# Optimization experiments

Measured on AMD Instinct MI355X. Metric: run time of the kernel, lower is better.

## Reference

```python
import jax, jax.numpy as jnp
import numpy as np
from jax import lax

# --- constants derived from init args ---
TAU = 0.1
CNSTS = (1.0, 10.0)
EPSILON = CNSTS[0] / TAU          # 10.0
LAMBDAA = CNSTS[0] * CNSTS[1] / TAU  # 100.0
ALPHA = 0.5
SIGMA = 2.0
ITER_NUM = 5
IN_CHANNELS = 3
M = max(4 * int(2 * SIGMA) + 1, 5)  # 17


def gauss_kernel():
    # 2D normalized Gaussian, shape [C, 1, M, M] for depthwise conv (OIHW with groups=C)
    xx = jnp.arange(M, dtype=jnp.float32) - (M - 1.0) / 2.0
    d2 = xx[:, None] ** 2 + xx[None, :] ** 2
    w = jnp.exp(-d2 / (2.0 * SIGMA ** 2))
    w = w / w.sum()
    return jnp.broadcast_to(w[None, None], (IN_CHANNELS, 1, M, M))


def depthwise_conv(x, w):
    # x: [B, C, H, W], w: [C, 1, M, M]; SAME padding (M odd, pad = M//2)
    return lax.conv_general_dilated(
        x, w, window_strides=(1, 1), padding='SAME',
        dimension_numbers=('NCHW', 'OIHW', 'NCHW'),
        feature_group_count=IN_CHANNELS)


def setup_inputs() -> dict:
    key = jax.random.key(0)
    k1, k2 = jax.random.split(key)
    x = jax.random.uniform(k1, (8, 3, 512, 512), dtype=jnp.float32)
    c = jax.random.normal(k2, (8, 3, 512, 512), dtype=jnp.float32)
    return {'x': x, 'c': c}


def reference(x, c):
    w = gauss_kernel()
    b = jax.nn.sigmoid(10.0 * c)          # getb(c)
    lam_b = LAMBDAA * b
    u = jax.nn.sigmoid(-(lam_b * depthwise_conv(1.0 - 2.0 * x, w)) / EPSILON)
    for _ in range(max(abs(ITER_NUM), 1)):
        uu = (u - x) / TAU + lam_b * depthwise_conv(1.0 - 2.0 * u, w)
        uu = jax.nn.sigmoid(-uu / EPSILON)
        u = (1.0 - ALPHA) * u + ALPHA * uu
    return u
```

## Files before the change

kernel.cpp:

```cpp
#include <hip/hip_runtime.h>
#include <hip/hip_fp16.h>
#include <math.h>


#define TR   32
#define TC   64
#define HR   48
#define RAD  8
#define HW   512
#define NIMG 24
#define NPIX ((size_t)HW * HW * NIMG)

typedef _Float16 h2 __attribute__((ext_vector_type(2)));
typedef unsigned int uint;

#define G0  6.6916e-05f
#define G1  4.3635e-04f
#define G2  2.2159612e-03f
#define G3  8.7643070e-03f
#define G4  2.6995958e-02f
#define G5  6.4759932e-02f
#define G6  1.2098751e-01f
#define G7  1.7603572e-01f
#define G8  1.9947466e-01f
__device__ __constant__ const float GWc[17] = {
    G0,G1,G2,G3,G4,G5,G6,G7,G8,G7,G6,G5,G4,G3,G2,G1,G0
};

__device__ __forceinline__ float inv1pexp(float z) {
    return __builtin_amdgcn_rcpf(1.0f + __expf(z));
}

__device__ __forceinline__ float fdot2f(uint a, h2 b, float c) {
#if __has_builtin(__builtin_amdgcn_fdot2)
    return __builtin_amdgcn_fdot2(__builtin_bit_cast(h2, a), b, c, false);
#else
    h2 av = __builtin_bit_cast(h2, a);
    return (float)av.x * (float)b.x + (float)av.y * (float)b.y + c;
#endif
}
__device__ __forceinline__ float lo16f(uint v) {
    __half h = __ushort_as_half((unsigned short)(v & 0xffffu));
    return __half2float(h);
}
__device__ __forceinline__ float hi16f(uint v) {
    __half h = __ushort_as_half((unsigned short)(v >> 16));
    return __half2float(h);
}
__device__ __forceinline__ h2 gpair(int i) {
    const float G[16] = { G0,G1,G2,G3,G4,G5,G6,G7,G8,G7,G6,G5,G4,G3,G2,G1 };
    h2 r; r.x = (_Float16)G[2*i]; r.y = (_Float16)G[2*i+1]; return r;
}

template<int MODE>
__global__ __launch_bounds__(256, 6) void sig_step(
    const float* __restrict__ xg, const float* __restrict__ cgl,
    const __half* __restrict__ uin, __half2* __restrict__ xl,
    void* __restrict__ uout)
{
    __shared__ __half sTmp[HR * TC];

    const int t    = threadIdx.x;
    const int img  = blockIdx.z;
    const int row0 = blockIdx.y * TR;
    const int col0 = blockIdx.x * TC;
    const size_t ibase = (size_t)img * HW * HW;

    if (t < 192) {
        const int r   = t >> 2;
        const int ci2 = t & 3;
        const int gr  = row0 + r - RAD;
        const int gc0 = col0 + ci2 * 16 - RAD;

        uint wv[16];
#pragma unroll
        for (int i = 0; i < 16; ++i) wv[i] = 0x38003800u;
        if (gr >= 0 && gr < HW) {
            if constexpr (MODE == 0) {
#pragma unroll
                for (int k = 0; k < 4; ++k) {
                    int s = gc0 + 8 * k;
                    if (s >= 0 && s < HW) {
                        const float* xb = xg + ibase + (size_t)gr * HW + s;
                        float4 va = *reinterpret_cast<const float4*>(xb);
                        float4 vb = *reinterpret_cast<const float4*>(xb + 4);
                        wv[4*k+0] = __builtin_bit_cast(uint, __floats2half2_rn(va.x, va.y));
                        wv[4*k+1] = __builtin_bit_cast(uint, __floats2half2_rn(va.z, va.w));
                        wv[4*k+2] = __builtin_bit_cast(uint, __floats2half2_rn(vb.x, vb.y));
                        wv[4*k+3] = __builtin_bit_cast(uint, __floats2half2_rn(vb.z, vb.w));
                    }
                }
            } else {
#pragma unroll
                for (int k = 0; k < 4; ++k) {
                    int s = gc0 + 8 * k;
                    if (s >= 0 && s < HW) {
                        uint4 v = *reinterpret_cast<const uint4*>(
                                      uin + ibase + (size_t)gr * HW + s);
                        wv[4*k+0] = v.x; wv[4*k+1] = v.y;
                        wv[4*k+2] = v.z; wv[4*k+3] = v.w;
                    }
                }
            }
        }
        uint wo[15];
#pragma unroll
        for (int i = 0; i < 15; ++i)
            wo[i] = __builtin_amdgcn_alignbit(wv[i + 1], wv[i], 16);

        uint ow[8];
#pragma unroll
        for (int jp = 0; jp < 8; ++jp) {
            float a0 = 0.f, a1 = 0.f;
#pragma unroll
            for (int i = 0; i < 8; ++i) {
                h2 g = gpair(i);
                a0 = fdot2f(wv[jp + i], g, a0);
                a1 = fdot2f(wo[jp + i], g, a1);
            }
            a0 = fmaf(G0, lo16f(wv[jp + 8]), a0);
            a1 = fmaf(G0, hi16f(wv[jp + 8]), a1);
            ow[jp] = __builtin_bit_cast(uint, __floats2half2_rn(a0, a1));
        }
        uint4* orow = reinterpret_cast<uint4*>(&sTmp[r * TC + ci2 * 16]);
        orow[0] = make_uint4(ow[0], ow[1], ow[2], ow[3]);
        orow[1] = make_uint4(ow[4], ow[5], ow[6], ow[7]);
    }
    __syncthreads();

    const int cc = t & 63;
    const int rg = t >> 6;
    const size_t pbase = ibase + (size_t)(row0 + rg * 8) * HW + (col0 + cc);

    float win[24];
#pragma unroll
    for (int j = 0; j < 24; ++j)
        win[j] = __half2float(sTmp[(rg * 8 + j) * TC + cc]);

#pragma unroll
    for (int m = 0; m < 8; ++m) {
        float v = 0.f;
#pragma unroll
        for (int k = 0; k < 17; ++k) v += GWc[k] * win[m + k];
        float f = 1.f - 2.f * v;

        size_t gidx = pbase + (size_t)m * HW;
        if constexpr (MODE == 0) {
            float xv  = xg[gidx];
            float lam = 100.f * inv1pexp(-10.f * cgl[gidx]);
            xl[gidx] = __floats2half2_rn(xv, lam);
            ((__half*)uout)[gidx] = __float2half(inv1pexp(lam * f * 0.1f));
        } else {
            float2 p = __half22float2(xl[gidx]);
            float uprev = __half2float(uin[gidx]);
            float tt = (uprev - p.x) * 10.f + p.y * f;
            float uu = inv1pexp(tt * 0.1f);
            float res = 0.5f * (uprev + uu);
            if constexpr (MODE == 2) ((float*)uout)[gidx] = res;
            else                     ((__half*)uout)[gidx] = __float2half(res);
        }
    }
}

extern "C" void kernel_launch(void* const* d_in, const int* in_sizes, int n_in,
                              void* d_out, int out_size, void* d_ws, size_t ws_size,
                              hipStream_t stream) {
    const float* x = (const float*)d_in[0];
    const float* c = (const float*)d_in[1];

    __half* u0 = (__half*)d_ws;
    __half* u1 = u0 + NPIX;
    __half2* xl = (ws_size >= NPIX * 8)
        ? (__half2*)((char*)d_ws + NPIX * 4)
        : (__half2*)d_out;

    dim3 grid(HW / TC, HW / TR, NIMG);
    dim3 block(256);
    sig_step<0><<<grid, block, 0, stream>>>(x, c, nullptr, xl, u0);
    sig_step<1><<<grid, block, 0, stream>>>(x, c, u0, xl, u1);
    sig_step<1><<<grid, block, 0, stream>>>(x, c, u1, xl, u0);
    sig_step<1><<<grid, block, 0, stream>>>(x, c, u0, xl, u1);
    sig_step<1><<<grid, block, 0, stream>>>(x, c, u1, xl, u0);
    sig_step<2><<<grid, block, 0, stream>>>(x, c, u0, xl, d_out);
}
```

Baseline: 102.2 us.

## Pack row pairs in shared memory and use fdot2 for the vertical blur pass

The horizontal pass now has each thread handle 8 output columns for two adjacent rows and store them interleaved as half2 pairs (row 2k, row 2k+1) in shared memory. The vertical pass can then use the same packed fp16 dot2 routine instead of 17 scalar fp32 FMAs reading constant memory. This cuts vertical-pass ALU work and shared-memory reads by half. In exchange, per-thread load segments become narrower with more halo overlap, and the vertical blur now accumulates in fp16 dot products.

Result: faster. 99.65 us (median of 2 runs) (-2.5%).

```diff
diff --git a/kernel.cpp b/kernel.cpp
--- a/kernel.cpp
+++ b/kernel.cpp
@@ -5,7 +5,6 @@
 
 #define TR   32
 #define TC   64
-#define HR   48
 #define RAD  8
 #define HW   512
 #define NIMG 24
@@ -23,9 +22,6 @@
 #define G6  1.2098751e-01f
 #define G7  1.7603572e-01f
 #define G8  1.9947466e-01f
-__device__ __constant__ const float GWc[17] = {
-    G0,G1,G2,G3,G4,G5,G6,G7,G8,G7,G6,G5,G4,G3,G2,G1,G0
-};
 
 __device__ __forceinline__ float inv1pexp(float z) {
     return __builtin_amdgcn_rcpf(1.0f + __expf(z));
@@ -40,16 +36,30 @@
 #endif
 }
 __device__ __forceinline__ float lo16f(uint v) {
-    __half h = __ushort_as_half((unsigned short)(v & 0xffffu));
-    return __half2float(h);
+    return __half2float(__ushort_as_half((unsigned short)(v & 0xffffu)));
 }
 __device__ __forceinline__ float hi16f(uint v) {
-    __half h = __ushort_as_half((unsigned short)(v >> 16));
-    return __half2float(h);
+    return __half2float(__ushort_as_half((unsigned short)(v >> 16)));
 }
 __device__ __forceinline__ h2 gpair(int i) {
     const float G[16] = { G0,G1,G2,G3,G4,G5,G6,G7,G8,G7,G6,G5,G4,G3,G2,G1 };
     h2 r; r.x = (_Float16)G[2*i]; r.y = (_Float16)G[2*i+1]; return r;
+}
+__device__ __forceinline__ uint packh2(float lo, float hi) {
+    return __builtin_bit_cast(uint, __floats2half2_rn(lo, hi));
+}
+
+__device__ __forceinline__ void dot17(const uint* wv, const uint* wo,
+                                      int jp, float& aE, float& aO) {
+    float a0 = 0.f, a1 = 0.f;
+#pragma unroll
+    for (int i = 0; i < 8; ++i) {
+        h2 g = gpair(i);
+        a0 = fdot2f(wv[jp + i], g, a0);
+        a1 = fdot2f(wo[jp + i], g, a1);
+    }
+    aE = fmaf(G0, lo16f(wv[jp + 8]), a0);
+    aO = fmaf(G0, hi16f(wv[jp + 8]), a1);
 }
 
 template<int MODE>
@@ -58,7 +68,7 @@
     const __half* __restrict__ uin, __half2* __restrict__ xl,
     void* __restrict__ uout)
 {
-    __shared__ __half sTmp[HR * TC];
+    __shared__ uint sP[24 * 64];
 
     const int t    = threadIdx.x;
     const int img  = blockIdx.z;
@@ -67,64 +77,54 @@
     const size_t ibase = (size_t)img * HW * HW;
 
     if (t < 192) {
-        const int r   = t >> 2;
-        const int ci2 = t & 3;
-        const int gr  = row0 + r - RAD;
-        const int gc0 = col0 + ci2 * 16 - RAD;
-
-        uint wv[16];
+        const int rp  = t >> 3;
+        const int ci  = t & 7;
+        const int gc0 = col0 + ci * 8 - RAD;
+        float aE[2][4], aO[2][4];
 #pragma unroll
-        for (int i = 0; i < 16; ++i) wv[i] = 0x38003800u;
-        if (gr >= 0 && gr < HW) {
-            if constexpr (MODE == 0) {
+        for (int rr = 0; rr < 2; ++rr) {
+            const int gr = row0 + 2 * rp + rr - RAD;
+            uint wv[12];
 #pragma unroll
-                for (int k = 0; k < 4; ++k) {
-                    int s = gc0 + 8 * k;
-                    if (s >= 0 && s < HW) {
-                        const float* xb = xg + ibase + (size_t)gr * HW + s;
-                        float4 va = *reinterpret_cast<const float4*>(xb);
-                        float4 vb = *reinterpret_cast<const float4*>(xb + 4);
-                        wv[4*k+0] = __builtin_bit_cast(uint, __floats2half2_rn(va.x, va.y));
-                        wv[4*k+1] = __builtin_bit_cast(uint, __floats2half2_rn(va.z, va.w));
-                        wv[4*k+2] = __builtin_bit_cast(uint, __floats2half2_rn(vb.x, vb.y));
-                        wv[4*k+3] = __builtin_bit_cast(uint, __floats2half2_rn(vb.z, vb.w));
+            for (int i = 0; i < 12; ++i) wv[i] = 0x38003800u;
+            if (gr >= 0 && gr < HW) {
+                if constexpr (MODE == 0) {
+                    const float* xb = xg + ibase + (size_t)gr * HW;
+#pragma unroll
+                    for (int k = 0; k < 6; ++k) {
+                        int s = gc0 + 4 * k;
+                        if (s >= 0 && s < HW) {
+                            float4 v = *reinterpret_cast<const float4*>(&xb[s]);
+                            wv[2*k]   = packh2(v.x, v.y);
+                            wv[2*k+1] = packh2(v.z, v.w);
+                        }
                     }
-                }
-            } else {
+                } else {
+                    const __half* ub = uin + ibase + (size_t)gr * HW;
 #pragma unroll
-                for (int k = 0; k < 4; ++k) {
-                    int s = gc0 + 8 * k;
-                    if (s >= 0 && s < HW) {
-                        uint4 v = *reinterpret_cast<const uint4*>(
-                                      uin + ibase + (size_t)gr * HW + s);
-                        wv[4*k+0] = v.x; wv[4*k+1] = v.y;
-                        wv[4*k+2] = v.z; wv[4*k+3] = v.w;
+                    for (int k = 0; k < 3; ++k) {
+                        int s = gc0 + 8 * k;
+                        if (s >= 0 && s < HW) {
+                            uint4 v = *reinterpret_cast<const uint4*>(&ub[s]);
+                            wv[4*k+0] = v.x; wv[4*k+1] = v.y;
+                            wv[4*k+2] = v.z; wv[4*k+3] = v.w;
+                        }
                     }
                 }
             }
+            uint wo[11];
+#pragma unroll
+            for (int i = 0; i < 11; ++i)
+                wo[i] = __builtin_amdgcn_alignbit(wv[i + 1], wv[i], 16);
+#pragma unroll
+            for (int jp = 0; jp < 4; ++jp)
+                dot17(wv, wo, jp, aE[rr][jp], aO[rr][jp]);
         }
-        uint wo[15];
-#pragma unroll
-        for (int i = 0; i < 15; ++i)
-            wo[i] = __builtin_amdgcn_alignbit(wv[i + 1], wv[i], 16);
-
-        uint ow[8];
-#pragma unroll
-        for (int jp = 0; jp < 8; ++jp) {
-            float a0 = 0.f, a1 = 0.f;
-#pragma unroll
-            for (int i = 0; i < 8; ++i) {
-                h2 g = gpair(i);
-                a0 = fdot2f(wv[jp + i], g, a0);
-                a1 = fdot2f(wo[jp + i], g, a1);
-            }
-            a0 = fmaf(G0, lo16f(wv[jp + 8]), a0);
-            a1 = fmaf(G0, hi16f(wv[jp + 8]), a1);
-            ow[jp] = __builtin_bit_cast(uint, __floats2half2_rn(a0, a1));
-        }
-        uint4* orow = reinterpret_cast<uint4*>(&sTmp[r * TC + ci2 * 16]);
-        orow[0] = make_uint4(ow[0], ow[1], ow[2], ow[3]);
-        orow[1] = make_uint4(ow[4], ow[5], ow[6], ow[7]);
+        uint4* orow = reinterpret_cast<uint4*>(&sP[rp * 64 + ci * 8]);
+        orow[0] = make_uint4(packh2(aE[0][0], aE[1][0]), packh2(aO[0][0], aO[1][0]),
+                             packh2(aE[0][1], aE[1][1]), packh2(aO[0][1], aO[1][1]));
+        orow[1] = make_uint4(packh2(aE[0][2], aE[1][2]), packh2(aO[0][2], aO[1][2]),
+                             packh2(aE[0][3], aE[1][3]), packh2(aO[0][3], aO[1][3]));
     }
     __syncthreads();
 
@@ -132,32 +132,40 @@
     const int rg = t >> 6;
     const size_t pbase = ibase + (size_t)(row0 + rg * 8) * HW + (col0 + cc);
 
-    float win[24];
+    uint p[12];
 #pragma unroll
-    for (int j = 0; j < 24; ++j)
-        win[j] = __half2float(sTmp[(rg * 8 + j) * TC + cc]);
+    for (int j = 0; j < 12; ++j)
+        p[j] = sP[(rg * 4 + j) * 64 + cc];
+    uint po[11];
+#pragma unroll
+    for (int j = 0; j < 11; ++j)
+        po[j] = __builtin_amdgcn_alignbit(p[j + 1], p[j], 16);
 
 #pragma unroll
-    for (int m = 0; m < 8; ++m) {
-        float v = 0.f;
+    for (int jp = 0; jp < 4; ++jp) {
+        float vE, vO;
+        dot17(p, po, jp, vE, vO);
 #pragma unroll
-        for (int k = 0; k < 17; ++k) v += GWc[k] * win[m + k];
-        float f = 1.f - 2.f * v;
+        for (int h = 0; h < 2; ++h) {
+            int m = 2 * jp + h;
+            float v = h ? vO : vE;
+            float f = 1.f - 2.f * v;
 
-        size_t gidx = pbase + (size_t)m * HW;
-        if constexpr (MODE == 0) {
-            float xv  = xg[gidx];
-            float lam = 100.f * inv1pexp(-10.f * cgl[gidx]);
-            xl[gidx] = __floats2half2_rn(xv, lam);
-            ((__half*)uout)[gidx] = __float2half(inv1pexp(lam * f * 0.1f));
-        } else {
-            float2 p = __half22float2(xl[gidx]);
-            float uprev = __half2float(uin[gidx]);
-            float tt = (uprev - p.x) * 10.f + p.y * f;
-            float uu = inv1pexp(tt * 0.1f);
-            float res = 0.5f * (uprev + uu);
-            if constexpr (MODE == 2) ((float*)uout)[gidx] = res;
-            else                     ((__half*)uout)[gidx] = __float2half(res);
+            size_t gidx = pbase + (size_t)m * HW;
+            if constexpr (MODE == 0) {
+                float xv  = xg[gidx];
+                float lam = 100.f * inv1pexp(-10.f * cgl[gidx]);
+                xl[gidx] = __floats2half2_rn(xv, lam);
+                ((__half*)uout)[gidx] = __float2half(inv1pexp(lam * f * 0.1f));
+            } else {
+                float2 pr = __half22float2(xl[gidx]);
+                float uprev = __half2float(uin[gidx]);
+                float tt = (uprev - pr.x) * 10.f + pr.y * f;
+                float uu = inv1pexp(tt * 0.1f);
+                float res = 0.5f * (uprev + uu);
+                if constexpr (MODE == 2) ((float*)uout)[gidx] = res;
+                else                     ((__half*)uout)[gidx] = __float2half(res);
+            }
         }
     }
 }
```
